# Kernel tuning notes

Measured on AMD Instinct MI355X. Metric: run time of the kernel, lower is better.

The kernel has to match this reference:

```python
import jax, jax.numpy as jnp
import numpy as np

B = 128        # graphs
NPG = 64       # nodes per graph (num_node)
N = B * NPG    # total nodes = 8192
IN = 16        # in_channels
D = 128        # d_model
OUT = 64       # out_channels
CAT = IN * NPG + NPG * NPG  # 5120
EPS = 1e-5


def _lin_init(k, fi, fo):
    s = 1.0 / np.sqrt(fi)
    kw, kb = jax.random.split(k)
    W = jax.random.uniform(kw, (fi, fo), jnp.float32, -s, s)
    b = jax.random.uniform(kb, (fo,), jnp.float32, -s, s)
    return W, b


def setup_inputs() -> dict:
    key = jax.random.key(0)
    ks = jax.random.split(key, 10)
    x = jax.random.normal(ks[0], (N, IN), jnp.float32)
    # complete graph (all i->j pairs, incl. self loops) per graph, offset per graph
    ii = np.repeat(np.arange(NPG), NPG)
    jj = np.tile(np.arange(NPG), NPG)
    off = (np.arange(B) * NPG)[:, None]
    row = (ii[None, :] + off).reshape(-1)
    col = (jj[None, :] + off).reshape(-1)
    edge_index = jnp.asarray(np.stack([row, col]), jnp.int32)  # [2, E]
    E = edge_index.shape[1]
    edge_weight = jax.random.uniform(ks[1], (E,), jnp.float32)
    batch = jnp.repeat(jnp.arange(B, dtype=jnp.int32), NPG)
    W1, b1 = _lin_init(ks[2], IN, D)
    W2, b2 = _lin_init(ks[3], D, D)
    Wm0, bm0 = _lin_init(ks[4], D + CAT, D)
    Wm1, bm1 = _lin_init(ks[5], D, D)
    Wm2, bm2 = _lin_init(ks[6], D, D)
    Wout, bout = _lin_init(ks[7], D, OUT)
    ones = jnp.ones((D,), jnp.float32)
    zeros = jnp.zeros((D,), jnp.float32)
    return dict(x=x, edge_index=edge_index, edge_weight=edge_weight, batch=batch,
                W1=W1, b1=b1, W2=W2, b2=b2,
                Wm0=Wm0, bm0=bm0, g0=ones, be0=zeros,
                Wm1=Wm1, bm1=bm1, g1=ones, be1=zeros,
                Wm2=Wm2, bm2=bm2, g2=ones, be2=zeros,
                Wout=Wout, bout=bout)


def _gcn_conv(h_in, row, col, ew, W, b):
    # PyG GCNConv: linear first, then D^-1/2 (A) D^-1/2 aggregation (self loops already present)
    h = h_in @ W                                             # [N, F]
    deg = jax.ops.segment_sum(ew, col, num_segments=N)       # in-degree by edge weight
    dinv = jnp.where(deg > 0, jax.lax.rsqrt(deg), 0.0)
    norm = dinv[row] * ew * dinv[col]                        # [E]
    out = jax.ops.segment_sum(norm[:, None] * h[row], col, num_segments=N)
    return out + b


def _bn(h, g, b):
    # BatchNorm1d, training-mode math (biased variance), eps=1e-5
    m = jnp.mean(h, axis=0)
    v = jnp.var(h, axis=0)
    return g * (h - m) * jax.lax.rsqrt(v + EPS) + b


def reference(x, edge_index, edge_weight, batch,
              W1, b1, W2, b2,
              Wm0, bm0, g0, be0,
              Wm1, bm1, g1, be1,
              Wm2, bm2, g2, be2,
              Wout, bout):
    row, col = edge_index[0], edge_index[1]
    h = _gcn_conv(x, row, col, edge_weight, W1, b1)
    h = jax.nn.relu(h)
    h = _gcn_conv(h, row, col, edge_weight, W2, b2)
    # global_mean_pool
    sums = jax.ops.segment_sum(h, batch, num_segments=B)
    cnt = jax.ops.segment_sum(jnp.ones((N,), h.dtype), batch, num_segments=B)
    pooled = sums / cnt[:, None]
    pooled = jax.nn.relu(pooled)
    feat = jnp.concatenate([pooled, x.reshape(B, -1), edge_weight.reshape(B, -1)], axis=1)
    feat = jax.nn.relu(feat)
    h = _bn(jax.nn.relu(feat @ Wm0 + bm0), g0, be0)
    h = _bn(jax.nn.relu(h @ Wm1 + bm1), g1, be1)
    h = _bn(jax.nn.relu(h @ Wm2 + bm2), g2, be2)
    return h @ Wout + bout
```

## Files before the change

kernel.cpp:

```cpp
#include <hip/hip_runtime.h>

#define NG 128
#define NPG 64
#define IN 16
#define DM 128
#define NOUT 64
#define EPG 4096
#define KC 32
#define NCHUNK 164
#define BN_EPS 1e-5f

__global__ __launch_bounds__(256) void k_conv1(
    const float* __restrict__ x, const float* __restrict__ ew,
    const float* __restrict__ W1, const float* __restrict__ b1,
    float* __restrict__ z, float* __restrict__ stats)
{
    __shared__ float ew_s[EPG];
    __shared__ float x_s[NPG * IN];
    __shared__ float W1h_s[IN * 64];
    __shared__ float P_s[NPG * 64];
    __shared__ float b1h_s[64];
    __shared__ float dinv_s[NPG];
    __shared__ float t_s[NPG];

    const int g = blockIdx.x >> 1, half = blockIdx.x & 1, t = threadIdx.x;
    const int fh0 = half * 64;
    if (blockIdx.x == 0) {
        for (int i = t; i < 768; i += 256) stats[i] = 0.f;
    }
    {
        const float4* ew4 = (const float4*)(ew + g * EPG);
        float4* ews4 = (float4*)ew_s;
        #pragma unroll
        for (int i = 0; i < 4; i++) ews4[t + 256 * i] = ew4[t + 256 * i];
        ((float4*)x_s)[t] = ((const float4*)(x + g * NPG * IN))[t];
    }
    for (int i = t; i < IN * 64; i += 256)
        W1h_s[i] = W1[(i >> 6) * DM + fh0 + (i & 63)];
    if (t < 64) b1h_s[t] = b1[fh0 + t];
    __syncthreads();

    if (t < NPG) {
        float s = 0.f;
        #pragma unroll 8
        for (int i = 0; i < NPG; i++) s += ew_s[i * NPG + t];
        dinv_s[t] = (s > 0.f) ? rsqrtf(s) : 0.f;
    }
    __syncthreads();

    {
        const int j = t & 63, q = t >> 6;
        const float dj = dinv_s[j];
        for (int i = q * 16; i < q * 16 + 16; i++) {
            float vv = ew_s[i * NPG + j] * dj;
            #pragma unroll
            for (int off = 32; off > 0; off >>= 1) vv += __shfl_down(vv, off, 64);
            if (j == 0) t_s[i] = dinv_s[i] * vv * (1.f / 64.f);
        }
    }

    {
        const int f = t & 63, ih = t >> 6;
        for (int i = ih * 16; i < ih * 16 + 16; i++) {
            float acc = 0.f;
            #pragma unroll
            for (int k = 0; k < IN; k++) acc += x_s[i * IN + k] * W1h_s[k * 64 + f];
            P_s[i * 64 + f] = acc;
        }
    }
    __syncthreads();

    for (int i = t; i < EPG; i += 256) ew_s[i] *= dinv_s[i >> 6];
    __syncthreads();

    {
        const int j = t & 63, q = t >> 6, fb = q * 16;
        float acc[16];
        #pragma unroll
        for (int u = 0; u < 16; u++) acc[u] = 0.f;
        for (int i = 0; i < NPG; i++) {
            const float w = ew_s[i * NPG + j];
            const float4* p4 = (const float4*)(P_s + i * 64 + fb);
            #pragma unroll
            for (int u4 = 0; u4 < 4; u4++) {
                float4 p = p4[u4];
                acc[4 * u4 + 0] += w * p.x;
                acc[4 * u4 + 1] += w * p.y;
                acc[4 * u4 + 2] += w * p.z;
                acc[4 * u4 + 3] += w * p.w;
            }
        }
        const float dj = dinv_s[j], tj = t_s[j];
        #pragma unroll
        for (int u = 0; u < 16; u++) {
            float h = fmaxf(dj * acc[u] + b1h_s[fb + u], 0.f);
            float zv = tj * h;
            #pragma unroll
            for (int off = 32; off > 0; off >>= 1) zv += __shfl_down(zv, off, 64);
            if (j == 0) z[g * DM + fh0 + fb + u] = zv;
        }
    }
}

__global__ __launch_bounds__(256) void k_gemm_part(
    const float* __restrict__ z, const float* __restrict__ x,
    const float* __restrict__ ew, const float* __restrict__ W2,
    const float* __restrict__ b2, const float* __restrict__ Wm0,
    float* __restrict__ part)
{
    __shared__ float a_s[KC * 132];
    __shared__ float b_s[KC * DM];
    __shared__ float z_s[DM * 129];
    __shared__ float W2_s[DM * 32];
    const int c = blockIdx.x, t = threadIdx.x;

    if (c < 4) {
        for (int it = 0; it < 64; it++) {
            int idx = it * 256 + t;
            z_s[(idx >> 7) * 129 + (idx & 127)] = z[idx];
        }
        for (int idx = t; idx < DM * 32; idx += 256)
            W2_s[idx] = W2[(idx >> 5) * DM + c * 32 + (idx & 31)];
        __syncthreads();
        const int gg = t >> 1, kh = t & 1, k0 = kh * 16;
        float acc[16];
        #pragma unroll
        for (int u = 0; u < 16; u++) acc[u] = 0.f;
        for (int kk = 0; kk < DM; kk++) {
            const float zv = z_s[gg * 129 + kk];
            const float4* w4 = (const float4*)(W2_s + kk * 32 + k0);
            #pragma unroll
            for (int u4 = 0; u4 < 4; u4++) {
                float4 w = w4[u4];
                acc[4 * u4 + 0] += zv * w.x;
                acc[4 * u4 + 1] += zv * w.y;
                acc[4 * u4 + 2] += zv * w.z;
                acc[4 * u4 + 3] += zv * w.w;
            }
        }
        #pragma unroll
        for (int u = 0; u < 16; u++)
            a_s[(k0 + u) * 132 + gg] = fmaxf(acc[u] + b2[c * 32 + k0 + u], 0.f);
    } else {
        const float* src; int stride, off;
        if (c < 36) { src = x;  stride = 1024; off = c * 32 - 128; }
        else        { src = ew; stride = 4096; off = c * 32 - 1152; }
        for (int idx = t; idx < 128 * KC; idx += 256) {
            int gg = idx >> 5, k = idx & 31;
            a_s[k * 132 + gg] = fmaxf(src[gg * stride + off + k], 0.f);
        }
    }
    for (int idx = t; idx < KC * DM; idx += 256)
        b_s[idx] = Wm0[c * (KC * DM) + idx];
    __syncthreads();

    const int tf = t & 15, tg = t >> 4;
    const int g0 = tg * 8, f0 = tf * 8;
    float acc[8][8];
    #pragma unroll
    for (int i = 0; i < 8; i++)
        #pragma unroll
        for (int jx = 0; jx < 8; jx++) acc[i][jx] = 0.f;

    #pragma unroll 4
    for (int k = 0; k < KC; k++) {
        const float4 a0 = *(const float4*)(a_s + k * 132 + g0);
        const float4 a1 = *(const float4*)(a_s + k * 132 + g0 + 4);
        const float4 c0 = *(const float4*)(b_s + k * DM + f0);
        const float4 c1 = *(const float4*)(b_s + k * DM + f0 + 4);
        const float av[8] = {a0.x, a0.y, a0.z, a0.w, a1.x, a1.y, a1.z, a1.w};
        const float bv[8] = {c0.x, c0.y, c0.z, c0.w, c1.x, c1.y, c1.z, c1.w};
        #pragma unroll
        for (int i = 0; i < 8; i++)
            #pragma unroll
            for (int jx = 0; jx < 8; jx++) acc[i][jx] += av[i] * bv[jx];
    }

    float* pp = part + c * 16384;
    #pragma unroll
    for (int i = 0; i < 8; i++) {
        float4* o = (float4*)(pp + (g0 + i) * 128 + f0);
        o[0] = make_float4(acc[i][0], acc[i][1], acc[i][2], acc[i][3]);
        o[1] = make_float4(acc[i][4], acc[i][5], acc[i][6], acc[i][7]);
    }
}

__global__ __launch_bounds__(256) void k_reduce_bn0(
    const float* __restrict__ part, const float* __restrict__ bm0,
    float* __restrict__ v0, float* __restrict__ stats0)
{
    const int bx = blockIdx.x, t = threadIdx.x;
    const int fgrp = bx & 7, gt = bx >> 3;
    const int fsub = t & 15, gl = (t >> 4) & 3, ch = t >> 6;
    const int f = fgrp * 16 + fsub, g = gt * 4 + gl;

    const float* p = part + g * 128 + f + (size_t)ch * 41 * 16384;
    float v = 0.f;
    #pragma unroll 8
    for (int cc = 0; cc < 41; cc++) v += p[cc * 16384];

    __shared__ float r1[256];
    r1[t] = v;
    __syncthreads();
    __shared__ float sv[64], sv2[64];
    if (ch == 0) {
        v = r1[t] + r1[t + 64] + r1[t + 128] + r1[t + 192] + bm0[f];
        v = fmaxf(v, 0.f);
        v0[g * 128 + f] = v;
        sv[t] = v; sv2[t] = v * v;
    }
    __syncthreads();
    if (t < 16) {
        float s1 = sv[t] + sv[t + 16] + sv[t + 32] + sv[t + 48];
        float s2 = sv2[t] + sv2[t + 16] + sv2[t + 32] + sv2[t + 48];
        atomicAdd(&stats0[(fgrp * 16 + t) * 2], s1);
        atomicAdd(&stats0[(fgrp * 16 + t) * 2 + 1], s2);
    }
}

__global__ __launch_bounds__(256) void k_mlp(
    const float* __restrict__ vin, const float* __restrict__ statsin,
    const float* __restrict__ gbn, const float* __restrict__ bbn,
    const float* __restrict__ W, const float* __restrict__ bias,
    float* __restrict__ vout, float* __restrict__ statsout)
{
    __shared__ float h_s[128 * 129];
    __shared__ float wcol[128];
    __shared__ float scale_s[128], shift_s[128];
    __shared__ float pc[128];
    __shared__ float rr[4];
    const int f = blockIdx.x, t = threadIdx.x;
    if (t < 128) {
        float s1 = statsin[t * 2], s2 = statsin[t * 2 + 1];
        float m = s1 * (1.f / 128.f);
        float var = s2 * (1.f / 128.f) - m * m;
        float sc = gbn[t] * rsqrtf(var + BN_EPS);
        scale_s[t] = sc;
        shift_s[t] = bbn[t] - m * sc;
        wcol[t] = W[t * 128 + f];
    }
    __syncthreads();
    #pragma unroll 4
    for (int it = 0; it < 64; it++) {
        int idx = it * 256 + t;
        int g = idx >> 7, k = idx & 127;
        h_s[g * 129 + k] = vin[idx] * scale_s[k] + shift_s[k];
    }
    __syncthreads();
    const int g = t & 127, kh = t >> 7;
    float acc = 0.f;
    #pragma unroll 8
    for (int k = kh * 64; k < kh * 64 + 64; k++) acc += h_s[g * 129 + k] * wcol[k];
    if (kh) pc[g] = acc;
    __syncthreads();
    if (t < 128) {
        float v = fmaxf(acc + pc[t] + bias[f], 0.f);
        vout[t * 128 + f] = v;
        float s1 = v, s2 = v * v;
        #pragma unroll
        for (int off = 32; off > 0; off >>= 1) {
            s1 += __shfl_down(s1, off, 64);
            s2 += __shfl_down(s2, off, 64);
        }
        if ((t & 63) == 0) { rr[(t >> 6) * 2] = s1; rr[(t >> 6) * 2 + 1] = s2; }
    }
    __syncthreads();
    if (t == 0) {
        statsout[f * 2]     = rr[0] + rr[2];
        statsout[f * 2 + 1] = rr[1] + rr[3];
    }
}

__global__ __launch_bounds__(128) void k_out(
    const float* __restrict__ vin, const float* __restrict__ statsin,
    const float* __restrict__ gbn, const float* __restrict__ bbn,
    const float* __restrict__ Wo, const float* __restrict__ bo,
    float* __restrict__ out)
{
    __shared__ float Wo_s[128 * 64];
    __shared__ float vrow[2][128];
    __shared__ float scale_s[128], shift_s[128];
    const int b = blockIdx.x, t = threadIdx.x, g0 = b * 2;
    {
        float s1 = statsin[t * 2], s2 = statsin[t * 2 + 1];
        float m = s1 * (1.f / 128.f);
        float var = s2 * (1.f / 128.f) - m * m;
        float sc = gbn[t] * rsqrtf(var + BN_EPS);
        scale_s[t] = sc;
        shift_s[t] = bbn[t] - m * sc;
    }
    __syncthreads();
    #pragma unroll 8
    for (int it = 0; it < 64; it++) {
        int idx = it * 128 + t;
        Wo_s[idx] = Wo[idx];
    }
    #pragma unroll
    for (int it = 0; it < 2; it++) {
        int idx = it * 128 + t;
        int g2 = idx >> 7, k = idx & 127;
        vrow[g2][k] = vin[(g0 + g2) * 128 + k] * scale_s[k] + shift_s[k];
    }
    __syncthreads();
    const int g2 = t >> 6, o = t & 63;
    float acc = bo[o];
    #pragma unroll 8
    for (int k = 0; k < 128; k++) acc += vrow[g2][k] * Wo_s[k * 64 + o];
    out[(g0 + g2) * NOUT + o] = acc;
}

extern "C" void kernel_launch(void* const* d_in, const int* in_sizes, int n_in,
                              void* d_out, int out_size, void* d_ws, size_t ws_size,
                              hipStream_t stream)
{
    const float* x   = (const float*)d_in[0];
    const float* ew  = (const float*)d_in[2];
    const float* W1  = (const float*)d_in[4];
    const float* b1  = (const float*)d_in[5];
    const float* W2  = (const float*)d_in[6];
    const float* b2  = (const float*)d_in[7];
    const float* Wm0 = (const float*)d_in[8];
    const float* bm0 = (const float*)d_in[9];
    const float* g0  = (const float*)d_in[10];
    const float* be0 = (const float*)d_in[11];
    const float* Wm1 = (const float*)d_in[12];
    const float* bm1 = (const float*)d_in[13];
    const float* g1  = (const float*)d_in[14];
    const float* be1 = (const float*)d_in[15];
    const float* Wm2 = (const float*)d_in[16];
    const float* bm2 = (const float*)d_in[17];
    const float* g2  = (const float*)d_in[18];
    const float* be2 = (const float*)d_in[19];
    const float* Wo  = (const float*)d_in[20];
    const float* bo  = (const float*)d_in[21];

    float* ws    = (float*)d_ws;
    float* zbuf  = ws;
    float* part  = zbuf + 16384;
    float* v0    = part + NCHUNK * 16384;
    float* v1    = v0 + 16384;
    float* v2    = v1 + 16384;
    float* stats = v2 + 16384;

    k_conv1<<<NG * 2, 256, 0, stream>>>(x, ew, W1, b1, zbuf, stats);
    k_gemm_part<<<NCHUNK, 256, 0, stream>>>(zbuf, x, ew, W2, b2, Wm0, part);
    k_reduce_bn0<<<256, 256, 0, stream>>>(part, bm0, v0, stats);
    k_mlp<<<128, 256, 0, stream>>>(v0, stats,       g0, be0, Wm1, bm1, v1, stats + 256);
    k_mlp<<<128, 256, 0, stream>>>(v1, stats + 256, g1, be1, Wm2, bm2, v2, stats + 512);
    k_out<<<NOUT, 128, 0, stream>>>(v2, stats + 512, g2, be2, Wo, bo, (float*)d_out);
}
```

Before: 160.2 us.

## Run raw-feature Wm0 GEMM concurrently with conv in one fused front kernel

The conv1 blocks and the part of the Wm0 GEMM that uses only x and edge_weight now share one launch, so the GEMM over the 5120 raw features runs alongside the graph convolution instead of after it. The pooled branch (z·W2 then the first 128 rows of Wm0) moves to a small separate kernel that runs after the front kernel. GEMM tiles change from 164 chunks of K=32 with all 128 outputs to 160 blocks of K=64 with half the outputs each, which halves the partial buffer the reduction has to read. The cost is a union shared-memory buffer sized for the larger branch, and the small pooled kernel has each block reload the full W2 and Wm0 head matrices.

```diff
diff --git a/kernel.cpp b/kernel.cpp
--- a/kernel.cpp
+++ b/kernel.cpp
@@ -6,207 +6,214 @@
 #define DM 128
 #define NOUT 64
 #define EPG 4096
-#define KC 32
-#define NCHUNK 164
+#define NGEMM 160
 #define BN_EPS 1e-5f
 
-__global__ __launch_bounds__(256) void k_conv1(
+__global__ __launch_bounds__(256) void k_front(
     const float* __restrict__ x, const float* __restrict__ ew,
     const float* __restrict__ W1, const float* __restrict__ b1,
-    float* __restrict__ z, float* __restrict__ stats)
-{
-    __shared__ float ew_s[EPG];
-    __shared__ float x_s[NPG * IN];
-    __shared__ float W1h_s[IN * 64];
-    __shared__ float P_s[NPG * 64];
-    __shared__ float b1h_s[64];
-    __shared__ float dinv_s[NPG];
-    __shared__ float t_s[NPG];
-
-    const int g = blockIdx.x >> 1, half = blockIdx.x & 1, t = threadIdx.x;
-    const int fh0 = half * 64;
-    if (blockIdx.x == 0) {
-        for (int i = t; i < 768; i += 256) stats[i] = 0.f;
-    }
-    {
-        const float4* ew4 = (const float4*)(ew + g * EPG);
-        float4* ews4 = (float4*)ew_s;
+    const float* __restrict__ Wm0,
+    float* __restrict__ z, float* __restrict__ part, float* __restrict__ stats)
+{
+    __shared__ float u[12544];
+    const int b = blockIdx.x, t = threadIdx.x;
+
+    if (b < 256) {
+        float* ew_s   = u;
+        float* x_s    = u + 4096;
+        float* W1h_s  = u + 5120;
+        float* P_s    = u + 6144;
+        float* b1h_s  = u + 10240;
+        float* dinv_s = u + 10304;
+        float* t_s    = u + 10368;
+        const int g = b >> 1, half = b & 1, fh0 = half * 64;
+        if (b == 0) {
+            for (int i = t; i < 768; i += 256) stats[i] = 0.f;
+        }
+        {
+            const float4* ew4 = (const float4*)(ew + g * EPG);
+            float4* ews4 = (float4*)ew_s;
+            #pragma unroll
+            for (int i = 0; i < 4; i++) ews4[t + 256 * i] = ew4[t + 256 * i];
+            ((float4*)x_s)[t] = ((const float4*)(x + g * NPG * IN))[t];
+        }
+        for (int i = t; i < IN * 64; i += 256)
+            W1h_s[i] = W1[(i >> 6) * DM + fh0 + (i & 63)];
+        if (t < 64) b1h_s[t] = b1[fh0 + t];
+        __syncthreads();
+
+        if (t < NPG) {
+            float s = 0.f;
+            #pragma unroll 8
+            for (int i = 0; i < NPG; i++) s += ew_s[i * NPG + t];
+            dinv_s[t] = (s > 0.f) ? rsqrtf(s) : 0.f;
+        }
+        __syncthreads();
+
+        {
+            const int j = t & 63, q = t >> 6;
+            const float dj = dinv_s[j];
+            for (int i = q * 16; i < q * 16 + 16; i++) {
+                float vv = ew_s[i * NPG + j] * dj;
+                #pragma unroll
+                for (int off = 32; off > 0; off >>= 1) vv += __shfl_down(vv, off, 64);
+                if (j == 0) t_s[i] = dinv_s[i] * vv * (1.f / 64.f);
+            }
+        }
+
+        {
+            const int f = t & 63, ih = t >> 6;
+            for (int i = ih * 16; i < ih * 16 + 16; i++) {
+                float acc = 0.f;
+                #pragma unroll
+                for (int k = 0; k < IN; k++) acc += x_s[i * IN + k] * W1h_s[k * 64 + f];
+                P_s[i * 64 + f] = acc;
+            }
+        }
+        __syncthreads();
+
+        for (int i = t; i < EPG; i += 256) ew_s[i] *= dinv_s[i >> 6];
+        __syncthreads();
+
+        {
+            const int j = t & 63, q = t >> 6, fb = q * 16;
+            float acc[16];
+            #pragma unroll
+            for (int uu = 0; uu < 16; uu++) acc[uu] = 0.f;
+            for (int i = 0; i < NPG; i++) {
+                const float w = ew_s[i * NPG + j];
+                const float4* p4 = (const float4*)(P_s + i * 64 + fb);
+                #pragma unroll
+                for (int u4 = 0; u4 < 4; u4++) {
+                    float4 p = p4[u4];
+                    acc[4 * u4 + 0] += w * p.x;
+                    acc[4 * u4 + 1] += w * p.y;
+                    acc[4 * u4 + 2] += w * p.z;
+                    acc[4 * u4 + 3] += w * p.w;
+                }
+            }
+            const float dj = dinv_s[j], tj = t_s[j];
+            #pragma unroll
+            for (int uu = 0; uu < 16; uu++) {
+                float h = fmaxf(dj * acc[uu] + b1h_s[fb + uu], 0.f);
+                float zv = tj * h;
+                #pragma unroll
+                for (int off = 32; off > 0; off >>= 1) zv += __shfl_down(zv, off, 64);
+                if (j == 0) z[g * DM + fh0 + fb + uu] = zv;
+            }
+        }
+    } else {
+        const int c = b - 256;
+        const int kc = c >> 1, fh = c & 1;
+        float* a_s = u;
+        float* b_s = u + 8448;
+
+        const float* src; int stride, off;
+        if (kc < 16) { src = x;  stride = 1024; off = kc * 64; }
+        else         { src = ew; stride = 4096; off = (kc - 16) * 64; }
+        const int K0 = 128 + kc * 64;
+
+        #pragma unroll 4
+        for (int it = 0; it < 32; it++) {
+            int idx = it * 256 + t;
+            int gg = idx >> 6, k = idx & 63;
+            a_s[k * 132 + gg] = fmaxf(src[gg * stride + off + k], 0.f);
+        }
+        #pragma unroll 4
+        for (int it = 0; it < 16; it++) {
+            int idx = it * 256 + t;
+            int k = idx >> 6, fl = idx & 63;
+            b_s[k * 64 + fl] = Wm0[(K0 + k) * 128 + fh * 64 + fl];
+        }
+        __syncthreads();
+
+        const int gthr = t & 31, fthr = t >> 5;
+        const int g0 = gthr * 4, f0 = fthr * 8;
+        float acc[4][8];
         #pragma unroll
-        for (int i = 0; i < 4; i++) ews4[t + 256 * i] = ew4[t + 256 * i];
-        ((float4*)x_s)[t] = ((const float4*)(x + g * NPG * IN))[t];
-    }
-    for (int i = t; i < IN * 64; i += 256)
-        W1h_s[i] = W1[(i >> 6) * DM + fh0 + (i & 63)];
-    if (t < 64) b1h_s[t] = b1[fh0 + t];
-    __syncthreads();
-
-    if (t < NPG) {
-        float s = 0.f;
-        #pragma unroll 8
-        for (int i = 0; i < NPG; i++) s += ew_s[i * NPG + t];
-        dinv_s[t] = (s > 0.f) ? rsqrtf(s) : 0.f;
-    }
-    __syncthreads();
-
-    {
-        const int j = t & 63, q = t >> 6;
-        const float dj = dinv_s[j];
-        for (int i = q * 16; i < q * 16 + 16; i++) {
-            float vv = ew_s[i * NPG + j] * dj;
-            #pragma unroll
-            for (int off = 32; off > 0; off >>= 1) vv += __shfl_down(vv, off, 64);
-            if (j == 0) t_s[i] = dinv_s[i] * vv * (1.f / 64.f);
-        }
-    }
-
-    {
-        const int f = t & 63, ih = t >> 6;
-        for (int i = ih * 16; i < ih * 16 + 16; i++) {
-            float acc = 0.f;
-            #pragma unroll
-            for (int k = 0; k < IN; k++) acc += x_s[i * IN + k] * W1h_s[k * 64 + f];
-            P_s[i * 64 + f] = acc;
-        }
-    }
-    __syncthreads();
-
-    for (int i = t; i < EPG; i += 256) ew_s[i] *= dinv_s[i >> 6];
-    __syncthreads();
-
-    {
-        const int j = t & 63, q = t >> 6, fb = q * 16;
-        float acc[16];
+        for (int i = 0; i < 4; i++)
+            #pragma unroll
+            for (int jx = 0; jx < 8; jx++) acc[i][jx] = 0.f;
+
+        #pragma unroll 4
+        for (int k = 0; k < 64; k++) {
+            const float4 a4  = *(const float4*)(a_s + k * 132 + g0);
+            const float4 c0v = *(const float4*)(b_s + k * 64 + f0);
+            const float4 c1v = *(const float4*)(b_s + k * 64 + f0 + 4);
+            const float av[4] = {a4.x, a4.y, a4.z, a4.w};
+            const float bv[8] = {c0v.x, c0v.y, c0v.z, c0v.w, c1v.x, c1v.y, c1v.z, c1v.w};
+            #pragma unroll
+            for (int i = 0; i < 4; i++)
+                #pragma unroll
+                for (int jx = 0; jx < 8; jx++) acc[i][jx] += av[i] * bv[jx];
+        }
+
+        float* pp = part + c * 8192;
         #pragma unroll
-        for (int u = 0; u < 16; u++) acc[u] = 0.f;
-        for (int i = 0; i < NPG; i++) {
-            const float w = ew_s[i * NPG + j];
-            const float4* p4 = (const float4*)(P_s + i * 64 + fb);
-            #pragma unroll
-            for (int u4 = 0; u4 < 4; u4++) {
-                float4 p = p4[u4];
-                acc[4 * u4 + 0] += w * p.x;
-                acc[4 * u4 + 1] += w * p.y;
-                acc[4 * u4 + 2] += w * p.z;
-                acc[4 * u4 + 3] += w * p.w;
-            }
-        }
-        const float dj = dinv_s[j], tj = t_s[j];
-        #pragma unroll
-        for (int u = 0; u < 16; u++) {
-            float h = fmaxf(dj * acc[u] + b1h_s[fb + u], 0.f);
-            float zv = tj * h;
-            #pragma unroll
-            for (int off = 32; off > 0; off >>= 1) zv += __shfl_down(zv, off, 64);
-            if (j == 0) z[g * DM + fh0 + fb + u] = zv;
-        }
-    }
-}
-
-__global__ __launch_bounds__(256) void k_gemm_part(
-    const float* __restrict__ z, const float* __restrict__ x,
-    const float* __restrict__ ew, const float* __restrict__ W2,
+        for (int i = 0; i < 4; i++) {
+            float4* o = (float4*)(pp + (g0 + i) * 64 + f0);
+            o[0] = make_float4(acc[i][0], acc[i][1], acc[i][2], acc[i][3]);
+            o[1] = make_float4(acc[i][4], acc[i][5], acc[i][6], acc[i][7]);
+        }
+    }
+}
+
+__global__ __launch_bounds__(256) void k_pooled(
+    const float* __restrict__ zbuf, const float* __restrict__ W2,
     const float* __restrict__ b2, const float* __restrict__ Wm0,
-    float* __restrict__ part)
-{
-    __shared__ float a_s[KC * 132];
-    __shared__ float b_s[KC * DM];
-    __shared__ float z_s[DM * 129];
-    __shared__ float W2_s[DM * 32];
-    const int c = blockIdx.x, t = threadIdx.x;
-
-    if (c < 4) {
-        for (int it = 0; it < 64; it++) {
-            int idx = it * 256 + t;
-            z_s[(idx >> 7) * 129 + (idx & 127)] = z[idx];
-        }
-        for (int idx = t; idx < DM * 32; idx += 256)
-            W2_s[idx] = W2[(idx >> 5) * DM + c * 32 + (idx & 31)];
-        __syncthreads();
-        const int gg = t >> 1, kh = t & 1, k0 = kh * 16;
-        float acc[16];
-        #pragma unroll
-        for (int u = 0; u < 16; u++) acc[u] = 0.f;
-        for (int kk = 0; kk < DM; kk++) {
-            const float zv = z_s[gg * 129 + kk];
-            const float4* w4 = (const float4*)(W2_s + kk * 32 + k0);
-            #pragma unroll
-            for (int u4 = 0; u4 < 4; u4++) {
-                float4 w = w4[u4];
-                acc[4 * u4 + 0] += zv * w.x;
-                acc[4 * u4 + 1] += zv * w.y;
-                acc[4 * u4 + 2] += zv * w.z;
-                acc[4 * u4 + 3] += zv * w.w;
-            }
-        }
-        #pragma unroll
-        for (int u = 0; u < 16; u++)
-            a_s[(k0 + u) * 132 + gg] = fmaxf(acc[u] + b2[c * 32 + k0 + u], 0.f);
-    } else {
-        const float* src; int stride, off;
-        if (c < 36) { src = x;  stride = 1024; off = c * 32 - 128; }
-        else        { src = ew; stride = 4096; off = c * 32 - 1152; }
-        for (int idx = t; idx < 128 * KC; idx += 256) {
-            int gg = idx >> 5, k = idx & 31;
-            a_s[k * 132 + gg] = fmaxf(src[gg * stride + off + k], 0.f);
-        }
-    }
-    for (int idx = t; idx < KC * DM; idx += 256)
-        b_s[idx] = Wm0[c * (KC * DM) + idx];
-    __syncthreads();
-
-    const int tf = t & 15, tg = t >> 4;
-    const int g0 = tg * 8, f0 = tf * 8;
-    float acc[8][8];
-    #pragma unroll
-    for (int i = 0; i < 8; i++)
-        #pragma unroll
-        for (int jx = 0; jx < 8; jx++) acc[i][jx] = 0.f;
-
-    #pragma unroll 4
-    for (int k = 0; k < KC; k++) {
-        const float4 a0 = *(const float4*)(a_s + k * 132 + g0);
-        const float4 a1 = *(const float4*)(a_s + k * 132 + g0 + 4);
-        const float4 c0 = *(const float4*)(b_s + k * DM + f0);
-        const float4 c1 = *(const float4*)(b_s + k * DM + f0 + 4);
-        const float av[8] = {a0.x, a0.y, a0.z, a0.w, a1.x, a1.y, a1.z, a1.w};
-        const float bv[8] = {c0.x, c0.y, c0.z, c0.w, c1.x, c1.y, c1.z, c1.w};
-        #pragma unroll
-        for (int i = 0; i < 8; i++)
-            #pragma unroll
-            for (int jx = 0; jx < 8; jx++) acc[i][jx] += av[i] * bv[jx];
-    }
-
-    float* pp = part + c * 16384;
-    #pragma unroll
-    for (int i = 0; i < 8; i++) {
-        float4* o = (float4*)(pp + (g0 + i) * 128 + f0);
-        o[0] = make_float4(acc[i][0], acc[i][1], acc[i][2], acc[i][3]);
-        o[1] = make_float4(acc[i][4], acc[i][5], acc[i][6], acc[i][7]);
-    }
+    float* __restrict__ pooled_part)
+{
+    __shared__ float W2_s[16384];
+    __shared__ float Wm0_s[16384];
+    __shared__ float z_s[256];
+    __shared__ float pooled_s[2 * 130];
+    const int bb = blockIdx.x, t = threadIdx.x, g0 = bb * 2;
+
+    for (int i = t; i < 4096; i += 256) {
+        ((float4*)W2_s)[i]  = ((const float4*)W2)[i];
+        ((float4*)Wm0_s)[i] = ((const float4*)Wm0)[i];
+    }
+    if (t < 64) ((float4*)z_s)[t] = ((const float4*)(zbuf + g0 * DM))[t];
+    __syncthreads();
+
+    const int cc = t & 127, r = t >> 7;
+    float acc = b2[cc];
+    #pragma unroll 8
+    for (int k = 0; k < DM; k++) acc += z_s[r * DM + k] * W2_s[k * DM + cc];
+    pooled_s[r * 130 + cc] = fmaxf(acc, 0.f);
+    __syncthreads();
+
+    float acc2 = 0.f;
+    #pragma unroll 8
+    for (int k = 0; k < DM; k++) acc2 += pooled_s[r * 130 + k] * Wm0_s[k * DM + cc];
+    pooled_part[(g0 + r) * DM + cc] = acc2;
 }
 
 __global__ __launch_bounds__(256) void k_reduce_bn0(
-    const float* __restrict__ part, const float* __restrict__ bm0,
-    float* __restrict__ v0, float* __restrict__ stats0)
+    const float* __restrict__ part, const float* __restrict__ pooled_part,
+    const float* __restrict__ bm0, float* __restrict__ v0,
+    float* __restrict__ stats0)
 {
     const int bx = blockIdx.x, t = threadIdx.x;
     const int fgrp = bx & 7, gt = bx >> 3;
     const int fsub = t & 15, gl = (t >> 4) & 3, ch = t >> 6;
     const int f = fgrp * 16 + fsub, g = gt * 4 + gl;
-
-    const float* p = part + g * 128 + f + (size_t)ch * 41 * 16384;
+    const int fh = f >> 6, fl = f & 63;
+
+    const float* p = part + (size_t)(2 * (ch * 20) + fh) * 8192 + g * 64 + fl;
     float v = 0.f;
-    #pragma unroll 8
-    for (int cc = 0; cc < 41; cc++) v += p[cc * 16384];
+    #pragma unroll 5
+    for (int cc = 0; cc < 20; cc++) v += p[(size_t)cc * 2 * 8192];
 
     __shared__ float r1[256];
     r1[t] = v;
     __syncthreads();
     __shared__ float sv[64], sv2[64];
     if (ch == 0) {
-        v = r1[t] + r1[t + 64] + r1[t + 128] + r1[t + 192] + bm0[f];
+        v = r1[t] + r1[t + 64] + r1[t + 128] + r1[t + 192]
+          + bm0[f] + pooled_part[g * DM + f];
         v = fmaxf(v, 0.f);
-        v0[g * 128 + f] = v;
+        v0[g * DM + f] = v;
         sv[t] = v; sv2[t] = v * v;
     }
     __syncthreads();
@@ -334,17 +341,18 @@
     const float* Wo  = (const float*)d_in[20];
     const float* bo  = (const float*)d_in[21];
 
-    float* ws    = (float*)d_ws;
-    float* zbuf  = ws;
-    float* part  = zbuf + 16384;
-    float* v0    = part + NCHUNK * 16384;
-    float* v1    = v0 + 16384;
-    float* v2    = v1 + 16384;
-    float* stats = v2 + 16384;
-
-    k_conv1<<<NG * 2, 256, 0, stream>>>(x, ew, W1, b1, zbuf, stats);
-    k_gemm_part<<<NCHUNK, 256, 0, stream>>>(zbuf, x, ew, W2, b2, Wm0, part);
-    k_reduce_bn0<<<256, 256, 0, stream>>>(part, bm0, v0, stats);
+    float* ws     = (float*)d_ws;
+    float* zbuf   = ws;
+    float* part   = zbuf + 16384;
+    float* ppart  = part + NGEMM * 8192;
+    float* v0     = ppart + 16384;
+    float* v1     = v0 + 16384;
+    float* v2     = v1 + 16384;
+    float* stats  = v2 + 16384;
+
+    k_front<<<256 + NGEMM, 256, 0, stream>>>(x, ew, W1, b1, Wm0, zbuf, part, stats);
+    k_pooled<<<64, 256, 0, stream>>>(zbuf, W2, b2, Wm0, ppart);
+    k_reduce_bn0<<<256, 256, 0, stream>>>(part, ppart, bm0, v0, stats);
     k_mlp<<<128, 256, 0, stream>>>(v0, stats,       g0, be0, Wm1, bm1, v1, stats + 256);
     k_mlp<<<128, 256, 0, stream>>>(v1, stats + 256, g1, be1, Wm2, bm2, v2, stats + 512);
     k_out<<<NOUT, 128, 0, stream>>>(v2, stats + 512, g2, be2, Wo, bo, (float*)d_out);
```

New measurement: 148.2 us. 7.5% less time.
